# Performance work log

Hardware: AMD Instinct MI355X
Metric: run time of the kernel (lower is better)

The kernel has to match this reference:

```python
import jax, jax.numpy as jnp
import numpy as np

B, N, M = 32, 512, 32          # batch frames, atoms, neighbors
H_A = 64                        # atom embedding dim
DMIN, DMAX, STEP = 0.0, 10.0, 0.1
FILTERS = jnp.arange(DMIN, DMAX + STEP, STEP, dtype=jnp.float32)  # [101]
H_B = FILTERS.shape[0]
N_CONV = 4
N_CLASSES = 10
BN_EPS = 1e-5


def setup_inputs() -> dict:
    key = jax.random.key(0)
    ks = jax.random.split(key, 6)
    return {
        "nbr_adj_dist": jax.random.uniform(ks[0], (B, N, M), jnp.float32) * DMAX,
        "nbr_adj_list": jax.random.randint(ks[1], (B, N, M), 0, N),
        "emb_w": jax.random.normal(ks[2], (N, H_A), jnp.float32),
        "fc_w": jax.random.normal(ks[3], (N_CONV, 2 * H_A + H_B, 2 * H_A), jnp.float32) * 0.05,
        "fc_b": jnp.zeros((N_CONV, 2 * H_A), jnp.float32),
        "bn1_g": jnp.ones((N_CONV, 2 * H_A), jnp.float32),
        "bn1_b": jnp.zeros((N_CONV, 2 * H_A), jnp.float32),
        "bn2_g": jnp.ones((N_CONV, H_A), jnp.float32),
        "bn2_b": jnp.zeros((N_CONV, H_A), jnp.float32),
        "cls_w": jax.random.normal(ks[4], (H_A, N_CLASSES), jnp.float32) * 0.05,
        "cls_b": jnp.zeros((N_CLASSES,), jnp.float32),
    }


def _bn(x2d, g, b):
    # training-mode BatchNorm1d over flattened batch axis (biased variance)
    mu = x2d.mean(axis=0)
    var = x2d.var(axis=0)
    return g * (x2d - mu) * jax.lax.rsqrt(var + BN_EPS) + b


def reference(nbr_adj_dist, nbr_adj_list, emb_w, fc_w, fc_b,
              bn1_g, bn1_b, bn2_g, bn2_b, cls_w, cls_b):
    # 1. Gaussian basis expansion of neighbor distances: [B,N,M,H_B]
    nbr_emb = jnp.exp(-((nbr_adj_dist[..., None] - FILTERS) ** 2) / (STEP ** 2))
    # 2. atom embeddings: atom_emb_idx = arange(N) per batch element
    atom = jnp.broadcast_to(emb_w[None], (B, N, H_A))
    # 3. CGCNN-style graph convolutions
    for l in range(N_CONV):
        # neighbor gather per batch: [B,N,M,H_A]
        nbrs = jax.vmap(lambda e, idx: e[idx])(atom, nbr_adj_list)
        total = jnp.concatenate(
            [jnp.broadcast_to(atom[:, :, None, :], (B, N, M, H_A)), nbrs, nbr_emb],
            axis=-1)                                        # [B,N,M,2*H_A+H_B]
        gated = jnp.einsum('bnmf,fh->bnmh', total, fc_w[l]) + fc_b[l]
        gated = _bn(gated.reshape(-1, 2 * H_A), bn1_g[l], bn1_b[l]).reshape(B, N, M, 2 * H_A)
        filt, core = jnp.split(gated, 2, axis=-1)
        summed = jnp.sum(jax.nn.sigmoid(filt) * jax.nn.relu(core), axis=2)  # [B,N,H_A]
        summed = _bn(summed.reshape(-1, H_A), bn2_g[l], bn2_b[l]).reshape(B, N, H_A)
        atom = jax.nn.relu(atom + summed)  # layer-internal residual
    # 4-6. activation, mean pooling over atoms, classifier, softmax
    emb = jax.nn.relu(atom)
    pooled = jnp.sum(emb, axis=1) / N                      # [B,H_A]
    logits = pooled @ cls_w + cls_b                        # [B,n_classes]
    return jax.nn.softmax(logits, axis=-1)
```

## Files before the change

### kernel.cpp

```cpp
#include <hip/hip_runtime.h>
#include <math.h>

typedef _Float16 half_t;
typedef __attribute__((ext_vector_type(4))) _Float16 half4;

constexpr int kB   = 32;
constexpr int kN   = 512;
constexpr int kM   = 32;
constexpr int kHA  = 64;
constexpr int kHB  = 101;
constexpr int kHO  = 128;
constexpr int kNF  = 229;
constexpr int kRows = kB * kN;
constexpr long kTRows = (long)kRows * kM;
constexpr int kNCls = 10;
constexpr float kEps = 1e-5f;
constexpr int kG    = 8;
constexpr int kNB   = kRows / kG;
constexpr int kT    = 512;
constexpr int kTaps = 8;

__device__ __forceinline__ int origCh(int j) {
    return ((j & 1) << 6) + ((j >> 2) << 1) + ((j >> 1) & 1);
}

__global__ void k_init_atom(const float* __restrict__ emb, float* __restrict__ atom) {
    int i = blockIdx.x * blockDim.x + threadIdx.x;
    atom[i] = emb[i & (kN * kHA - 1)];
}

template<bool RESID>
__global__ __launch_bounds__(256)
void k_pre(const float* __restrict__ atomIn, float* __restrict__ atomOut,
           const float* __restrict__ summed, const float* __restrict__ acc2,
           const float* __restrict__ g2, const float* __restrict__ b2,
           const float* __restrict__ W, const float* __restrict__ bias,
           float* __restrict__ preA, float* __restrict__ preB,
           float* __restrict__ bn1acc, float* __restrict__ zeroBuf) {
    __shared__ float sA[32 * 64];
    __shared__ float sc2s[128];
    int t = threadIdx.x;
    if (blockIdx.x == 0) {
        bn1acc[t] = 0.f;
        if (t < 128) zeroBuf[t] = 0.f;
    }
    if (RESID) {
        if (t < 64) {
            float inv = 1.f / (float)kRows;
            float mu = acc2[t] * inv;
            float var = acc2[64 + t] * inv - mu * mu;
            float sc = g2[t] * rsqrtf(var + kEps);
            sc2s[t] = sc;
            sc2s[64 + t] = b2[t] - mu * sc;
        }
        __syncthreads();
    }
    int r0 = blockIdx.x * 32;
    for (int i = t; i < 32 * 64; i += 256) {
        float v = atomIn[r0 * 64 + i];
        if (RESID) {
            int h = i & 63;
            v = fmaxf(v + fmaf(summed[r0 * 64 + i], sc2s[h], sc2s[64 + h]), 0.f);
            atomOut[r0 * 64 + i] = v;
        }
        sA[i] = v;
    }
    __syncthreads();
    int cg = t & 31, rg = t >> 5;
    float2 bb01 = *(const float2*)&bias[2 * cg];
    float2 bb23 = *(const float2*)&bias[64 + 2 * cg];
    float4 accA[4], accB[4];
    #pragma unroll
    for (int r = 0; r < 4; ++r) {
        accA[r] = make_float4(bb01.x, bb23.x, bb01.y, bb23.y);
        accB[r] = make_float4(0.f, 0.f, 0.f, 0.f);
    }
    for (int k = 0; k < 64; ++k) {
        float2 wA01 = *(const float2*)&W[k * kHO + 2 * cg];
        float2 wA23 = *(const float2*)&W[k * kHO + 64 + 2 * cg];
        float2 wB01 = *(const float2*)&W[(64 + k) * kHO + 2 * cg];
        float2 wB23 = *(const float2*)&W[(64 + k) * kHO + 64 + 2 * cg];
        #pragma unroll
        for (int r = 0; r < 4; ++r) {
            float a = sA[(rg * 4 + r) * 64 + k];
            accA[r].x = fmaf(a, wA01.x, accA[r].x);
            accA[r].y = fmaf(a, wA23.x, accA[r].y);
            accA[r].z = fmaf(a, wA01.y, accA[r].z);
            accA[r].w = fmaf(a, wA23.y, accA[r].w);
            accB[r].x = fmaf(a, wB01.x, accB[r].x);
            accB[r].y = fmaf(a, wB23.x, accB[r].y);
            accB[r].z = fmaf(a, wB01.y, accB[r].z);
            accB[r].w = fmaf(a, wB23.y, accB[r].w);
        }
    }
    #pragma unroll
    for (int r = 0; r < 4; ++r) {
        int row = r0 + rg * 4 + r;
        *(float4*)&preA[row * kHO + 4 * cg] = accA[r];
        *(float4*)&preB[row * kHO + 4 * cg] = accB[r];
    }
}

__global__ __launch_bounds__(kT, 6)
void k_stats(const float* __restrict__ dist, const int* __restrict__ nbrs,
             const float* __restrict__ preA, const float* __restrict__ preB,
             const float* __restrict__ W3, float* __restrict__ acc) {
    __shared__ half_t W3h[kHB * kHO];
    __shared__ float wv[kG][kM][kTaps];
    __shared__ int   roff[kG][kM];
    __shared__ int   wbase[kG][kM];
    __shared__ float red[2048];
    int t = threadIdx.x;
    int lb = (int)(blockIdx.x & 7) * (kNB / 8) + (int)(blockIdx.x >> 3);
    for (int i = t; i < kHB * kHO; i += kT)
        W3h[i] = (half_t)W3[(i & ~127) + origCh(i & 127)];
    if (t < kG * kM) {
        int g = t >> 5, m = t & 31;
        int p = lb * kG + g;
        float d = dist[p * kM + m];
        int kc = (int)floorf(d * 10.f);
        int ks = min(max(kc - 3, 0), kHB - kTaps);
        wbase[g][m] = ks * kHO;
        roff[g][m] = (((p >> 9) << 9) + nbrs[p * kM + m]) * kHO;
        #pragma unroll
        for (int j = 0; j < kTaps; ++j) {
            float dd = d - 0.1f * (float)(ks + j);
            wv[g][m][j] = __expf(-100.f * dd * dd);
        }
    }
    __syncthreads();
    int cg = t & 31, ms = t >> 5;
    float S[4] = {0.f, 0.f, 0.f, 0.f}, SS[4] = {0.f, 0.f, 0.f, 0.f};
    for (int g = 0; g < kG; ++g) {
        int p = lb * kG + g;
        float4 pa = *(const float4*)&preA[p * kHO + 4 * cg];
        #pragma unroll
        for (int mm = 0; mm < 2; ++mm) {
            int m = ms + mm * 16;
            int ro = roff[g][m], wb = wbase[g][m];
            float4 pb = *(const float4*)&preB[ro + 4 * cg];
            float x0 = pa.x + pb.x, x1 = pa.y + pb.y;
            float x2 = pa.z + pb.z, x3 = pa.w + pb.w;
            float warr[kTaps];
            *(float4*)&warr[0] = *(const float4*)&wv[g][m][0];
            *(float4*)&warr[4] = *(const float4*)&wv[g][m][4];
            const half_t* hb = &W3h[wb + 4 * cg];
            #pragma unroll
            for (int j = 0; j < kTaps; ++j) {
                half4 hv = *(const half4*)&hb[j * kHO];
                float w = warr[j];
                x0 = fmaf(w, (float)hv.x, x0);
                x1 = fmaf(w, (float)hv.y, x1);
                x2 = fmaf(w, (float)hv.z, x2);
                x3 = fmaf(w, (float)hv.w, x3);
            }
            S[0] += x0; S[1] += x1; S[2] += x2; S[3] += x3;
            SS[0] = fmaf(x0, x0, SS[0]); SS[1] = fmaf(x1, x1, SS[1]);
            SS[2] = fmaf(x2, x2, SS[2]); SS[3] = fmaf(x3, x3, SS[3]);
        }
    }
    #pragma unroll
    for (int c = 0; c < 4; ++c) {
        S[c]  += __shfl_xor(S[c], 32);
        SS[c] += __shfl_xor(SS[c], 32);
    }
    int w = t >> 6;
    if ((t & 63) < 32) {
        *(float4*)&red[w * 128 + cg * 4] = make_float4(S[0], S[1], S[2], S[3]);
        *(float4*)&red[1024 + w * 128 + cg * 4] = make_float4(SS[0], SS[1], SS[2], SS[3]);
    }
    __syncthreads();
    if (t < 256) {
        int j = t & 127, sel = t >> 7;
        float s = 0.f;
        #pragma unroll
        for (int ww = 0; ww < 8; ++ww) s += red[sel * 1024 + ww * 128 + j];
        atomicAdd(&acc[sel * 128 + j], s);
    }
}

__global__ __launch_bounds__(kT, 6)
void k_apply(const float* __restrict__ dist, const int* __restrict__ nbrs,
             const float* __restrict__ preA, const float* __restrict__ preB,
             const float* __restrict__ W3, const float* __restrict__ acc,
             const float* __restrict__ g1, const float* __restrict__ b1,
             float* __restrict__ summed, float* __restrict__ acc2) {
    __shared__ __align__(16) unsigned char smem[33792];
    __shared__ float wv[kG][kM][kTaps];
    __shared__ int   roff[kG][kM];
    __shared__ int   wbase[kG][kM];
    __shared__ float scP[128], shP[128];
    half_t* W3h = (half_t*)smem;
    float*  red = (float*)smem;
    int t = threadIdx.x;
    int lb = (int)(blockIdx.x & 7) * (kNB / 8) + (int)(blockIdx.x >> 3);
    for (int i = t; i < kHB * kHO; i += kT)
        W3h[i] = (half_t)W3[(i & ~127) + origCh(i & 127)];
    if (t < kG * kM) {
        int g = t >> 5, m = t & 31;
        int p = lb * kG + g;
        float d = dist[p * kM + m];
        int kc = (int)floorf(d * 10.f);
        int ks = min(max(kc - 3, 0), kHB - kTaps);
        wbase[g][m] = ks * kHO;
        roff[g][m] = (((p >> 9) << 9) + nbrs[p * kM + m]) * kHO;
        #pragma unroll
        for (int j = 0; j < kTaps; ++j) {
            float dd = d - 0.1f * (float)(ks + j);
            wv[g][m][j] = __expf(-100.f * dd * dd);
        }
    }
    if (t < 128) {
        float inv = 1.f / (float)kTRows;
        int oc = origCh(t);
        float mu = acc[t] * inv;
        float var = acc[128 + t] * inv - mu * mu;
        float sc = g1[oc] * rsqrtf(var + kEps);
        scP[t] = sc;
        shP[t] = b1[oc] - mu * sc;
    }
    __syncthreads();
    int cg = t & 31, ms = t >> 5;
    float4 sc4 = *(const float4*)&scP[4 * cg];
    float4 sh4 = *(const float4*)&shP[4 * cg];
    float s0g[kG], s1g[kG];
    #pragma unroll
    for (int g = 0; g < kG; ++g) { s0g[g] = 0.f; s1g[g] = 0.f; }
    #pragma unroll
    for (int g = 0; g < kG; ++g) {
        int p = lb * kG + g;
        float4 pa = *(const float4*)&preA[p * kHO + 4 * cg];
        #pragma unroll
        for (int mm = 0; mm < 2; ++mm) {
            int m = ms + mm * 16;
            int ro = roff[g][m], wb = wbase[g][m];
            float4 pb = *(const float4*)&preB[ro + 4 * cg];
            float x0 = pa.x + pb.x, x1 = pa.y + pb.y;
            float x2 = pa.z + pb.z, x3 = pa.w + pb.w;
            float warr[kTaps];
            *(float4*)&warr[0] = *(const float4*)&wv[g][m][0];
            *(float4*)&warr[4] = *(const float4*)&wv[g][m][4];
            const half_t* hb = &W3h[wb + 4 * cg];
            #pragma unroll
            for (int j = 0; j < kTaps; ++j) {
                half4 hv = *(const half4*)&hb[j * kHO];
                float w = warr[j];
                x0 = fmaf(w, (float)hv.x, x0);
                x1 = fmaf(w, (float)hv.y, x1);
                x2 = fmaf(w, (float)hv.z, x2);
                x3 = fmaf(w, (float)hv.w, x3);
            }
            float yf0 = fmaf(x0, sc4.x, sh4.x);
            float yc0 = fmaf(x1, sc4.y, sh4.y);
            float yf1 = fmaf(x2, sc4.z, sh4.z);
            float yc1 = fmaf(x3, sc4.w, sh4.w);
            float sg0 = 1.f / (1.f + __expf(-yf0));
            float sg1 = 1.f / (1.f + __expf(-yf1));
            s0g[g] = fmaf(sg0, fmaxf(yc0, 0.f), s0g[g]);
            s1g[g] = fmaf(sg1, fmaxf(yc1, 0.f), s1g[g]);
        }
    }
    __syncthreads();
    #pragma unroll
    for (int g = 0; g < kG; ++g)
        *(float2*)&red[(g * 16 + ms) * 64 + 2 * cg] = make_float2(s0g[g], s1g[g]);
    __syncthreads();
    int gg = t >> 6, ch = t & 63;
    float v = 0.f;
    #pragma unroll
    for (int m2 = 0; m2 < 16; ++m2) v += red[(gg * 16 + m2) * 64 + ch];
    summed[(size_t)(lb * kG + gg) * kHA + ch] = v;
    __syncthreads();
    red[t] = v;
    __syncthreads();
    if (t < 64) {
        float S2 = 0.f, SS2 = 0.f;
        #pragma unroll
        for (int g = 0; g < kG; ++g) {
            float u = red[g * 64 + t];
            S2 += u;
            SS2 = fmaf(u, u, SS2);
        }
        atomicAdd(&acc2[t], S2);
        atomicAdd(&acc2[64 + t], SS2);
    }
}

__global__ __launch_bounds__(1024)
void k_final(const float* __restrict__ atom, const float* __restrict__ summed,
             const float* __restrict__ acc2, const float* __restrict__ g2,
             const float* __restrict__ b2, const float* __restrict__ cw,
             const float* __restrict__ cb, float* __restrict__ out) {
    __shared__ float red[1024];
    __shared__ float sc2s[128];
    __shared__ float pooled[kHA];
    __shared__ float lg[kNCls];
    int b = blockIdx.x, t = threadIdx.x;
    if (t < 64) {
        float inv = 1.f / (float)kRows;
        float mu = acc2[t] * inv;
        float var = acc2[64 + t] * inv - mu * mu;
        float sc = g2[t] * rsqrtf(var + kEps);
        sc2s[t] = sc;
        sc2s[64 + t] = b2[t] - mu * sc;
    }
    __syncthreads();
    int h = t & 63, q = t >> 6;
    const float* ab = atom + (long)b * kN * kHA;
    const float* sb = summed + (long)b * kN * kHA;
    float scv = sc2s[h], shv = sc2s[64 + h];
    float s = 0.f;
    for (int n = q * 32; n < q * 32 + 32; ++n) {
        float v = ab[n * 64 + h] + fmaf(sb[n * 64 + h], scv, shv);
        s += fmaxf(v, 0.f);
    }
    red[t] = s;
    __syncthreads();
    if (t < 64) {
        float v = 0.f;
        #pragma unroll
        for (int qq = 0; qq < 16; ++qq) v += red[qq * 64 + t];
        pooled[t] = v * (1.f / kN);
    }
    __syncthreads();
    if (t < kNCls) {
        float a = cb[t];
        #pragma unroll
        for (int k = 0; k < kHA; ++k) a = fmaf(pooled[k], cw[k * kNCls + t], a);
        lg[t] = a;
    }
    __syncthreads();
    if (t == 0) {
        float mx = lg[0];
        for (int c = 1; c < kNCls; ++c) mx = fmaxf(mx, lg[c]);
        float e[kNCls], se = 0.f;
        for (int c = 0; c < kNCls; ++c) { e[c] = __expf(lg[c] - mx); se += e[c]; }
        float inv = 1.f / se;
        for (int c = 0; c < kNCls; ++c) out[b * kNCls + c] = e[c] * inv;
    }
}

extern "C" void kernel_launch(void* const* d_in, const int* in_sizes, int n_in,
                              void* d_out, int out_size, void* d_ws, size_t ws_size,
                              hipStream_t stream) {
    const float* dist = (const float*)d_in[0];
    const int*   nbrs = (const int*)d_in[1];
    const float* emb  = (const float*)d_in[2];
    const float* fcw  = (const float*)d_in[3];
    const float* fcb  = (const float*)d_in[4];
    const float* bn1g = (const float*)d_in[5];
    const float* bn1b = (const float*)d_in[6];
    const float* bn2g = (const float*)d_in[7];
    const float* bn2b = (const float*)d_in[8];
    const float* clw  = (const float*)d_in[9];
    const float* clb  = (const float*)d_in[10];
    float* out = (float*)d_out;

    float* ws     = (float*)d_ws;
    float* atom   = ws;
    float* preA   = atom + kRows * kHA;
    float* preB   = preA + kRows * kHO;
    float* summed = preB + kRows * kHO;
    float* bn1acc = summed + kRows * kHA;
    float* acc2a  = bn1acc + 256;
    float* acc2b  = acc2a + 128;

    k_init_atom<<<dim3(kRows * kHA / 256), dim3(256), 0, stream>>>(emb, atom);
    for (int l = 0; l < 4; ++l) {
        const float* W  = fcw + (long)l * kNF * kHO;
        const float* W3 = W + 2 * kHA * kHO;
        float* accW = (l & 1) ? acc2b : acc2a;
        float* accR = ((l - 1) & 1) ? acc2b : acc2a;
        if (l == 0)
            k_pre<false><<<dim3(kRows / 32), dim3(256), 0, stream>>>(
                atom, atom, nullptr, nullptr, nullptr, nullptr,
                W, fcb + l * kHO, preA, preB, bn1acc, accW);
        else
            k_pre<true><<<dim3(kRows / 32), dim3(256), 0, stream>>>(
                atom, atom, summed, accR, bn2g + (l - 1) * kHA, bn2b + (l - 1) * kHA,
                W, fcb + l * kHO, preA, preB, bn1acc, accW);
        k_stats<<<dim3(kNB), dim3(kT), 0, stream>>>(dist, nbrs, preA, preB, W3, bn1acc);
        k_apply<<<dim3(kNB), dim3(kT), 0, stream>>>(dist, nbrs, preA, preB, W3, bn1acc,
                                                    bn1g + l * kHO, bn1b + l * kHO,
                                                    summed, accW);
    }
    k_final<<<dim3(kB), dim3(1024), 0, stream>>>(atom, summed, acc2b,
                                                 bn2g + 3 * kHA, bn2b + 3 * kHA,
                                                 clw, clb, out);
}
```

Measured before the change: 727.7 us.

## Cache Gaussian-filter contributions in fp16 during stats pass for reuse in apply

The stats kernel now writes the per-edge Gaussian basis × W3 contribution (128 channels) to a half-precision workspace buffer. A new apply kernel reads that buffer instead of recomputing the 8-tap sparse dot product and rebuilding the fp16 W3 tile in shared memory. This trades recompute and shared-memory setup for writing and reading about 128 MB of fp16 traffic per layer. It also adds fp16 rounding of the cached term, and the path is taken only when the workspace is large enough.

```diff
diff --git a/kernel.cpp b/kernel.cpp
--- a/kernel.cpp
+++ b/kernel.cpp
@@ -101,10 +101,12 @@
     }
 }
 
+template<bool STORE_TS>
 __global__ __launch_bounds__(kT, 6)
 void k_stats(const float* __restrict__ dist, const int* __restrict__ nbrs,
              const float* __restrict__ preA, const float* __restrict__ preB,
-             const float* __restrict__ W3, float* __restrict__ acc) {
+             const float* __restrict__ W3, float* __restrict__ acc,
+             half_t* __restrict__ xh) {
     __shared__ half_t W3h[kHB * kHO];
     __shared__ float wv[kG][kM][kTaps];
     __shared__ int   roff[kG][kM];
@@ -139,21 +141,28 @@
             int m = ms + mm * 16;
             int ro = roff[g][m], wb = wbase[g][m];
             float4 pb = *(const float4*)&preB[ro + 4 * cg];
-            float x0 = pa.x + pb.x, x1 = pa.y + pb.y;
-            float x2 = pa.z + pb.z, x3 = pa.w + pb.w;
             float warr[kTaps];
             *(float4*)&warr[0] = *(const float4*)&wv[g][m][0];
             *(float4*)&warr[4] = *(const float4*)&wv[g][m][4];
+            float t0 = 0.f, t1 = 0.f, t2 = 0.f, t3 = 0.f;
             const half_t* hb = &W3h[wb + 4 * cg];
             #pragma unroll
             for (int j = 0; j < kTaps; ++j) {
                 half4 hv = *(const half4*)&hb[j * kHO];
                 float w = warr[j];
-                x0 = fmaf(w, (float)hv.x, x0);
-                x1 = fmaf(w, (float)hv.y, x1);
-                x2 = fmaf(w, (float)hv.z, x2);
-                x3 = fmaf(w, (float)hv.w, x3);
+                t0 = fmaf(w, (float)hv.x, t0);
+                t1 = fmaf(w, (float)hv.y, t1);
+                t2 = fmaf(w, (float)hv.z, t2);
+                t3 = fmaf(w, (float)hv.w, t3);
             }
+            if (STORE_TS) {
+                half4 hv4;
+                hv4.x = (half_t)t0; hv4.y = (half_t)t1;
+                hv4.z = (half_t)t2; hv4.w = (half_t)t3;
+                *(half4*)&xh[(size_t)(p * kM + m) * kHO + 4 * cg] = hv4;
+            }
+            float x0 = pa.x + pb.x + t0, x1 = pa.y + pb.y + t1;
+            float x2 = pa.z + pb.z + t2, x3 = pa.w + pb.w + t3;
             S[0] += x0; S[1] += x1; S[2] += x2; S[3] += x3;
             SS[0] = fmaf(x0, x0, SS[0]); SS[1] = fmaf(x1, x1, SS[1]);
             SS[2] = fmaf(x2, x2, SS[2]); SS[3] = fmaf(x3, x3, SS[3]);
@@ -176,6 +185,88 @@
         #pragma unroll
         for (int ww = 0; ww < 8; ++ww) s += red[sel * 1024 + ww * 128 + j];
         atomicAdd(&acc[sel * 128 + j], s);
+    }
+}
+
+__global__ __launch_bounds__(kT, 6)
+void k_apply_c(const int* __restrict__ nbrs,
+               const float* __restrict__ preA, const float* __restrict__ preB,
+               const half_t* __restrict__ xh, const float* __restrict__ acc,
+               const float* __restrict__ g1, const float* __restrict__ b1,
+               float* __restrict__ summed, float* __restrict__ acc2) {
+    __shared__ float red[kG * 16 * 64];
+    __shared__ int   roff[kG][kM];
+    __shared__ float scP[128], shP[128];
+    int t = threadIdx.x;
+    int lb = (int)(blockIdx.x & 7) * (kNB / 8) + (int)(blockIdx.x >> 3);
+    if (t < kG * kM) {
+        int g = t >> 5, m = t & 31;
+        int p = lb * kG + g;
+        roff[g][m] = (((p >> 9) << 9) + nbrs[p * kM + m]) * kHO;
+    }
+    if (t < 128) {
+        float inv = 1.f / (float)kTRows;
+        int oc = origCh(t);
+        float mu = acc[t] * inv;
+        float var = acc[128 + t] * inv - mu * mu;
+        float sc = g1[oc] * rsqrtf(var + kEps);
+        scP[t] = sc;
+        shP[t] = b1[oc] - mu * sc;
+    }
+    __syncthreads();
+    int cg = t & 31, ms = t >> 5;
+    float4 sc4 = *(const float4*)&scP[4 * cg];
+    float4 sh4 = *(const float4*)&shP[4 * cg];
+    float s0g[kG], s1g[kG];
+    #pragma unroll
+    for (int g = 0; g < kG; ++g) { s0g[g] = 0.f; s1g[g] = 0.f; }
+    #pragma unroll
+    for (int g = 0; g < kG; ++g) {
+        int p = lb * kG + g;
+        float4 pa = *(const float4*)&preA[p * kHO + 4 * cg];
+        #pragma unroll
+        for (int mm = 0; mm < 2; ++mm) {
+            int m = ms + mm * 16;
+            int ro = roff[g][m];
+            float4 pb = *(const float4*)&preB[ro + 4 * cg];
+            half4 tv = *(const half4*)&xh[(size_t)(p * kM + m) * kHO + 4 * cg];
+            float x0 = pa.x + pb.x + (float)tv.x;
+            float x1 = pa.y + pb.y + (float)tv.y;
+            float x2 = pa.z + pb.z + (float)tv.z;
+            float x3 = pa.w + pb.w + (float)tv.w;
+            float yf0 = fmaf(x0, sc4.x, sh4.x);
+            float yc0 = fmaf(x1, sc4.y, sh4.y);
+            float yf1 = fmaf(x2, sc4.z, sh4.z);
+            float yc1 = fmaf(x3, sc4.w, sh4.w);
+            float sg0 = 1.f / (1.f + __expf(-yf0));
+            float sg1 = 1.f / (1.f + __expf(-yf1));
+            s0g[g] = fmaf(sg0, fmaxf(yc0, 0.f), s0g[g]);
+            s1g[g] = fmaf(sg1, fmaxf(yc1, 0.f), s1g[g]);
+        }
+    }
+    __syncthreads();
+    #pragma unroll
+    for (int g = 0; g < kG; ++g)
+        *(float2*)&red[(g * 16 + ms) * 64 + 2 * cg] = make_float2(s0g[g], s1g[g]);
+    __syncthreads();
+    int gg = t >> 6, ch = t & 63;
+    float v = 0.f;
+    #pragma unroll
+    for (int m2 = 0; m2 < 16; ++m2) v += red[(gg * 16 + m2) * 64 + ch];
+    summed[(size_t)(lb * kG + gg) * kHA + ch] = v;
+    __syncthreads();
+    red[t] = v;
+    __syncthreads();
+    if (t < 64) {
+        float S2 = 0.f, SS2 = 0.f;
+        #pragma unroll
+        for (int g = 0; g < kG; ++g) {
+            float u = red[g * 64 + t];
+            S2 += u;
+            SS2 = fmaf(u, u, SS2);
+        }
+        atomicAdd(&acc2[t], S2);
+        atomicAdd(&acc2[64 + t], SS2);
     }
 }
 
@@ -364,6 +455,9 @@
     float* bn1acc = summed + kRows * kHA;
     float* acc2a  = bn1acc + 256;
     float* acc2b  = acc2a + 128;
+    half_t* xh    = (half_t*)(acc2b + 128);
+    size_t need   = (size_t)((char*)(xh + (size_t)kTRows * kHO) - (char*)d_ws);
+    const bool cached = ws_size >= need;
 
     k_init_atom<<<dim3(kRows * kHA / 256), dim3(256), 0, stream>>>(emb, atom);
     for (int l = 0; l < 4; ++l) {
@@ -379,10 +473,19 @@
             k_pre<true><<<dim3(kRows / 32), dim3(256), 0, stream>>>(
                 atom, atom, summed, accR, bn2g + (l - 1) * kHA, bn2b + (l - 1) * kHA,
                 W, fcb + l * kHO, preA, preB, bn1acc, accW);
-        k_stats<<<dim3(kNB), dim3(kT), 0, stream>>>(dist, nbrs, preA, preB, W3, bn1acc);
-        k_apply<<<dim3(kNB), dim3(kT), 0, stream>>>(dist, nbrs, preA, preB, W3, bn1acc,
-                                                    bn1g + l * kHO, bn1b + l * kHO,
-                                                    summed, accW);
+        if (cached) {
+            k_stats<true><<<dim3(kNB), dim3(kT), 0, stream>>>(
+                dist, nbrs, preA, preB, W3, bn1acc, xh);
+            k_apply_c<<<dim3(kNB), dim3(kT), 0, stream>>>(
+                nbrs, preA, preB, xh, bn1acc,
+                bn1g + l * kHO, bn1b + l * kHO, summed, accW);
+        } else {
+            k_stats<false><<<dim3(kNB), dim3(kT), 0, stream>>>(
+                dist, nbrs, preA, preB, W3, bn1acc, nullptr);
+            k_apply<<<dim3(kNB), dim3(kT), 0, stream>>>(
+                dist, nbrs, preA, preB, W3, bn1acc,
+                bn1g + l * kHO, bn1b + l * kHO, summed, accW);
+        }
     }
     k_final<<<dim3(kB), dim3(1024), 0, stream>>>(atom, summed, acc2b,
                                                  bn2g + 3 * kHA, bn2b + 3 * kHA,
```

New measurement: 892.6 us. +22.7%, slower.

## Replace per-edge Gaussian filter projection with interpolated precomputed distance table

Applied to the files above, without the earlier changes.

Adds a per-layer kernel that tabulates the Gaussian-basis projection W3·rbf(d) at 4097 distance samples, using 13 taps, and stores it in fp16. The stats and apply kernels then do linear interpolation between two table rows instead of staging the whole W3 matrix into shared memory and running an 8-tap FMA loop for each edge. This removes the per-block W3 load and conversion and most of the per-edge arithmetic, and it frees shared memory. The cost is interpolation error and two gathered global loads per edge from a 1 MB table.

```diff
diff --git a/kernel.cpp b/kernel.cpp
--- a/kernel.cpp
+++ b/kernel.cpp
@@ -18,7 +18,7 @@
 constexpr int kG    = 8;
 constexpr int kNB   = kRows / kG;
 constexpr int kT    = 512;
-constexpr int kTaps = 8;
+constexpr int kS    = 4096;
 
 __device__ __forceinline__ int origCh(int j) {
     return ((j & 1) << 6) + ((j >> 2) << 1) + ((j >> 1) & 1);
@@ -101,32 +101,46 @@
     }
 }
 
+__global__ __launch_bounds__(128)
+void k_table(const float* __restrict__ W3, half_t* __restrict__ tab) {
+    __shared__ float wv[13];
+    int s = blockIdx.x;
+    int t = threadIdx.x;
+    float d = (float)s * (10.f / (float)kS);
+    int kc = (int)floorf(d * 10.f);
+    int ks = min(max(kc - 6, 0), kHB - 13);
+    if (t < 13) {
+        float dd = d - 0.1f * (float)(ks + t);
+        wv[t] = __expf(-100.f * dd * dd);
+    }
+    __syncthreads();
+    int oc = origCh(t);
+    float a = 0.f;
+    #pragma unroll
+    for (int j = 0; j < 13; ++j)
+        a = fmaf(wv[j], W3[(ks + j) * kHO + oc], a);
+    tab[s * kHO + t] = (half_t)a;
+}
+
 __global__ __launch_bounds__(kT, 6)
 void k_stats(const float* __restrict__ dist, const int* __restrict__ nbrs,
              const float* __restrict__ preA, const float* __restrict__ preB,
-             const float* __restrict__ W3, float* __restrict__ acc) {
-    __shared__ half_t W3h[kHB * kHO];
-    __shared__ float wv[kG][kM][kTaps];
+             const half_t* __restrict__ tab, float* __restrict__ acc) {
     __shared__ int   roff[kG][kM];
-    __shared__ int   wbase[kG][kM];
+    __shared__ int   soff[kG][kM];
+    __shared__ float sfrac[kG][kM];
     __shared__ float red[2048];
     int t = threadIdx.x;
     int lb = (int)(blockIdx.x & 7) * (kNB / 8) + (int)(blockIdx.x >> 3);
-    for (int i = t; i < kHB * kHO; i += kT)
-        W3h[i] = (half_t)W3[(i & ~127) + origCh(i & 127)];
     if (t < kG * kM) {
         int g = t >> 5, m = t & 31;
         int p = lb * kG + g;
         float d = dist[p * kM + m];
-        int kc = (int)floorf(d * 10.f);
-        int ks = min(max(kc - 3, 0), kHB - kTaps);
-        wbase[g][m] = ks * kHO;
+        float sf = d * ((float)kS / 10.f);
+        int s = min((int)sf, kS - 1);
+        soff[g][m] = s * kHO;
+        sfrac[g][m] = sf - (float)s;
         roff[g][m] = (((p >> 9) << 9) + nbrs[p * kM + m]) * kHO;
-        #pragma unroll
-        for (int j = 0; j < kTaps; ++j) {
-            float dd = d - 0.1f * (float)(ks + j);
-            wv[g][m][j] = __expf(-100.f * dd * dd);
-        }
     }
     __syncthreads();
     int cg = t & 31, ms = t >> 5;
@@ -137,23 +151,18 @@
         #pragma unroll
         for (int mm = 0; mm < 2; ++mm) {
             int m = ms + mm * 16;
-            int ro = roff[g][m], wb = wbase[g][m];
+            int ro = roff[g][m], so = soff[g][m];
+            float fr = sfrac[g][m];
             float4 pb = *(const float4*)&preB[ro + 4 * cg];
-            float x0 = pa.x + pb.x, x1 = pa.y + pb.y;
-            float x2 = pa.z + pb.z, x3 = pa.w + pb.w;
-            float warr[kTaps];
-            *(float4*)&warr[0] = *(const float4*)&wv[g][m][0];
-            *(float4*)&warr[4] = *(const float4*)&wv[g][m][4];
-            const half_t* hb = &W3h[wb + 4 * cg];
-            #pragma unroll
-            for (int j = 0; j < kTaps; ++j) {
-                half4 hv = *(const half4*)&hb[j * kHO];
-                float w = warr[j];
-                x0 = fmaf(w, (float)hv.x, x0);
-                x1 = fmaf(w, (float)hv.y, x1);
-                x2 = fmaf(w, (float)hv.z, x2);
-                x3 = fmaf(w, (float)hv.w, x3);
-            }
+            half4 lo = *(const half4*)&tab[so + 4 * cg];
+            half4 hi = *(const half4*)&tab[so + kHO + 4 * cg];
+            float l0 = (float)lo.x, l1 = (float)lo.y, l2 = (float)lo.z, l3 = (float)lo.w;
+            float t0 = fmaf(fr, (float)hi.x - l0, l0);
+            float t1 = fmaf(fr, (float)hi.y - l1, l1);
+            float t2 = fmaf(fr, (float)hi.z - l2, l2);
+            float t3 = fmaf(fr, (float)hi.w - l3, l3);
+            float x0 = pa.x + pb.x + t0, x1 = pa.y + pb.y + t1;
+            float x2 = pa.z + pb.z + t2, x3 = pa.w + pb.w + t3;
             S[0] += x0; S[1] += x1; S[2] += x2; S[3] += x3;
             SS[0] = fmaf(x0, x0, SS[0]); SS[1] = fmaf(x1, x1, SS[1]);
             SS[2] = fmaf(x2, x2, SS[2]); SS[3] = fmaf(x3, x3, SS[3]);
@@ -182,33 +191,25 @@
 __global__ __launch_bounds__(kT, 6)
 void k_apply(const float* __restrict__ dist, const int* __restrict__ nbrs,
              const float* __restrict__ preA, const float* __restrict__ preB,
-             const float* __restrict__ W3, const float* __restrict__ acc,
+             const half_t* __restrict__ tab, const float* __restrict__ acc,
              const float* __restrict__ g1, const float* __restrict__ b1,
              float* __restrict__ summed, float* __restrict__ acc2) {
-    __shared__ __align__(16) unsigned char smem[33792];
-    __shared__ float wv[kG][kM][kTaps];
+    __shared__ float red[kG * 16 * 64];
     __shared__ int   roff[kG][kM];
-    __shared__ int   wbase[kG][kM];
+    __shared__ int   soff[kG][kM];
+    __shared__ float sfrac[kG][kM];
     __shared__ float scP[128], shP[128];
-    half_t* W3h = (half_t*)smem;
-    float*  red = (float*)smem;
     int t = threadIdx.x;
     int lb = (int)(blockIdx.x & 7) * (kNB / 8) + (int)(blockIdx.x >> 3);
-    for (int i = t; i < kHB * kHO; i += kT)
-        W3h[i] = (half_t)W3[(i & ~127) + origCh(i & 127)];
     if (t < kG * kM) {
         int g = t >> 5, m = t & 31;
         int p = lb * kG + g;
         float d = dist[p * kM + m];
-        int kc = (int)floorf(d * 10.f);
-        int ks = min(max(kc - 3, 0), kHB - kTaps);
-        wbase[g][m] = ks * kHO;
+        float sf = d * ((float)kS / 10.f);
+        int s = min((int)sf, kS - 1);
+        soff[g][m] = s * kHO;
+        sfrac[g][m] = sf - (float)s;
         roff[g][m] = (((p >> 9) << 9) + nbrs[p * kM + m]) * kHO;
-        #pragma unroll
-        for (int j = 0; j < kTaps; ++j) {
-            float dd = d - 0.1f * (float)(ks + j);
-            wv[g][m][j] = __expf(-100.f * dd * dd);
-        }
     }
     if (t < 128) {
         float inv = 1.f / (float)kTRows;
@@ -233,23 +234,18 @@
         #pragma unroll
         for (int mm = 0; mm < 2; ++mm) {
             int m = ms + mm * 16;
-            int ro = roff[g][m], wb = wbase[g][m];
+            int ro = roff[g][m], so = soff[g][m];
+            float fr = sfrac[g][m];
             float4 pb = *(const float4*)&preB[ro + 4 * cg];
-            float x0 = pa.x + pb.x, x1 = pa.y + pb.y;
-            float x2 = pa.z + pb.z, x3 = pa.w + pb.w;
-            float warr[kTaps];
-            *(float4*)&warr[0] = *(const float4*)&wv[g][m][0];
-            *(float4*)&warr[4] = *(const float4*)&wv[g][m][4];
-            const half_t* hb = &W3h[wb + 4 * cg];
-            #pragma unroll
-            for (int j = 0; j < kTaps; ++j) {
-                half4 hv = *(const half4*)&hb[j * kHO];
-                float w = warr[j];
-                x0 = fmaf(w, (float)hv.x, x0);
-                x1 = fmaf(w, (float)hv.y, x1);
-                x2 = fmaf(w, (float)hv.z, x2);
-                x3 = fmaf(w, (float)hv.w, x3);
-            }
+            half4 lo = *(const half4*)&tab[so + 4 * cg];
+            half4 hi = *(const half4*)&tab[so + kHO + 4 * cg];
+            float l0 = (float)lo.x, l1 = (float)lo.y, l2 = (float)lo.z, l3 = (float)lo.w;
+            float t0 = fmaf(fr, (float)hi.x - l0, l0);
+            float t1 = fmaf(fr, (float)hi.y - l1, l1);
+            float t2 = fmaf(fr, (float)hi.z - l2, l2);
+            float t3 = fmaf(fr, (float)hi.w - l3, l3);
+            float x0 = pa.x + pb.x + t0, x1 = pa.y + pb.y + t1;
+            float x2 = pa.z + pb.z + t2, x3 = pa.w + pb.w + t3;
             float yf0 = fmaf(x0, sc4.x, sh4.x);
             float yc0 = fmaf(x1, sc4.y, sh4.y);
             float yf1 = fmaf(x2, sc4.z, sh4.z);
@@ -364,6 +360,7 @@
     float* bn1acc = summed + kRows * kHA;
     float* acc2a  = bn1acc + 256;
     float* acc2b  = acc2a + 128;
+    half_t* tab   = (half_t*)(acc2b + 128);
 
     k_init_atom<<<dim3(kRows * kHA / 256), dim3(256), 0, stream>>>(emb, atom);
     for (int l = 0; l < 4; ++l) {
@@ -379,8 +376,9 @@
             k_pre<true><<<dim3(kRows / 32), dim3(256), 0, stream>>>(
                 atom, atom, summed, accR, bn2g + (l - 1) * kHA, bn2b + (l - 1) * kHA,
                 W, fcb + l * kHO, preA, preB, bn1acc, accW);
-        k_stats<<<dim3(kNB), dim3(kT), 0, stream>>>(dist, nbrs, preA, preB, W3, bn1acc);
-        k_apply<<<dim3(kNB), dim3(kT), 0, stream>>>(dist, nbrs, preA, preB, W3, bn1acc,
+        k_table<<<dim3(kS + 1), dim3(128), 0, stream>>>(W3, tab);
+        k_stats<<<dim3(kNB), dim3(kT), 0, stream>>>(dist, nbrs, preA, preB, tab, bn1acc);
+        k_apply<<<dim3(kNB), dim3(kT), 0, stream>>>(dist, nbrs, preA, preB, tab, bn1acc,
                                                     bn1g + l * kHO, bn1b + l * kHO,
                                                     summed, accW);
     }
```

Measured after the change: 747.6 us. 1.03x slower.
